# Kernel optimization log

Measured on AMD Instinct MI355X. Metric: run time of the kernel, lower is better.

The kernel has to match this reference:

```python
import jax, jax.numpy as jnp
import numpy as np

N_NODES = 50000
N_EDGES = 800000
IN_CH = 256
HID = 512
NUM_LAYERS = 3
EPS = 1e-12  # F.normalize eps


def setup_inputs() -> dict:
    key = jax.random.key(0)
    ks = jax.random.split(key, 2 + 3 * NUM_LAYERS)
    x = jax.random.normal(ks[0], (N_NODES, IN_CH), dtype=jnp.float32)
    edge_index = jax.random.randint(ks[1], (2, N_EDGES), 0, N_NODES, dtype=jnp.int64)
    inp = {"x": x, "edge_index": edge_index}
    dims = [(IN_CH, HID)] + [(HID, HID)] * (NUM_LAYERS - 1)
    for i, (din, dout) in enumerate(dims):
        s = 1.0 / np.sqrt(din)
        inp[f"Wl{i}"] = jax.random.normal(ks[2 + 3 * i], (din, dout), dtype=jnp.float32) * s
        inp[f"bl{i}"] = jnp.zeros((dout,), dtype=jnp.float32)
        inp[f"Wr{i}"] = jax.random.normal(ks[3 + 3 * i], (din, dout), dtype=jnp.float32) * s
    return inp


def _sage_conv(x, src, dst, Wl, bl, Wr):
    # aggr='add': out[dst] += x[src], then lin_l(agg) + lin_r(x), L2 normalize rows
    agg = jax.ops.segment_sum(x[src], dst, num_segments=x.shape[0])  # [N, din]
    out = agg @ Wl + bl + x @ Wr  # [N, dout]
    norm = jnp.maximum(jnp.linalg.norm(out, axis=-1, keepdims=True), EPS)
    return out / norm


def reference(x, edge_index, Wl0, bl0, Wr0, Wl1, bl1, Wr1, Wl2, bl2, Wr2):
    src, dst = edge_index[0], edge_index[1]
    feat = x
    params = [(Wl0, bl0, Wr0), (Wl1, bl1, Wr1), (Wl2, bl2, Wr2)]
    for Wl, bl, Wr in params:
        aggre = _sage_conv(feat, src, dst, Wl, bl, Wr)
        # Dropout(p=0.15) is identity in eval mode
        feat = jax.nn.elu(aggre)
    return feat
```

## Files before the change

### kernel.cpp

```cpp
#include <hip/hip_runtime.h>
#include <math.h>

#define N_NODES 50000
#define M_PAD   50048
#define N_EDGES 800000
#define HID 512

typedef short bf16x8 __attribute__((ext_vector_type(8)));
typedef float f32x4  __attribute__((ext_vector_type(4)));
typedef unsigned short u16x4 __attribute__((ext_vector_type(4)));

__device__ inline float b2f(unsigned short u) {
    union { unsigned int i; float f; } v; v.i = ((unsigned int)u) << 16; return v.f;
}
__device__ inline unsigned short f2b(float f) {
    union { float f; unsigned int i; } v; v.f = f;
    unsigned int r = v.i + 0x7FFFu + ((v.i >> 16) & 1u);
    return (unsigned short)(r >> 16);
}


__global__ void zero_kernel(int* __restrict__ p, int n) {
    int i = blockIdx.x * blockDim.x + threadIdx.x;
    if (i < n) p[i] = 0;
}

__global__ void detect_kernel(const int* __restrict__ e, int* __restrict__ flag) {
    if (blockIdx.x == 0 && threadIdx.x == 0) {
        int is64 = 1;
        for (int i = 0; i < 16; ++i)
            if (e[2 * i + 1] != 0) is64 = 0;
        *flag = is64;
    }
}

__global__ void hist_kernel(const void* __restrict__ eidx, const int* __restrict__ flag,
                            int* __restrict__ counts) {
    int e = blockIdx.x * blockDim.x + threadIdx.x;
    if (e >= N_EDGES) return;
    int is64 = *flag;
    int d;
    if (is64) d = (int)((const long long*)eidx)[N_EDGES + e];
    else      d = ((const int*)eidx)[N_EDGES + e];
    atomicAdd(&counts[d], 1);
}

__global__ __launch_bounds__(1024) void scan_kernel(const int* __restrict__ counts,
                                                    int* __restrict__ offsets) {
    __shared__ int sums[1024];
    int t = threadIdx.x;
    const int CH = (N_NODES + 1023) / 1024;
    int lo = t * CH;
    int hi = min(lo + CH, N_NODES);
    int s = 0;
    for (int i = lo; i < hi; ++i) s += counts[i];
    sums[t] = s;
    __syncthreads();
    for (int off = 1; off < 1024; off <<= 1) {
        int v = 0;
        if (t >= off) v = sums[t - off];
        __syncthreads();
        sums[t] += v;
        __syncthreads();
    }
    int excl = (t == 0) ? 0 : sums[t - 1];
    for (int i = lo; i < hi; ++i) { offsets[i] = excl; excl += counts[i]; }
    if (t == 1023) offsets[N_NODES] = excl;
}

__global__ void fill_kernel(const void* __restrict__ eidx, const int* __restrict__ flag,
                            const int* __restrict__ offsets, int* __restrict__ cursor,
                            int* __restrict__ edge_src) {
    int e = blockIdx.x * blockDim.x + threadIdx.x;
    if (e >= N_EDGES) return;
    int is64 = *flag;
    int s, d;
    if (is64) {
        const long long* p = (const long long*)eidx;
        s = (int)p[e];
        d = (int)p[N_EDGES + e];
    } else {
        const int* p = (const int*)eidx;
        s = p[e];
        d = p[N_EDGES + e];
    }
    int pos = atomicAdd(&cursor[d], 1);
    edge_src[offsets[d] + pos] = s;
}


__global__ __launch_bounds__(256) void xconv_kernel(const float* __restrict__ x,
                                                    unsigned short* __restrict__ cat1) {
    int id = blockIdx.x * 256 + threadIdx.x;
    if (id >= M_PAD * 64) return;
    int row = id >> 6;
    int c = (id & 63) * 4;
    float4 v = make_float4(0.f, 0.f, 0.f, 0.f);
    if (row < N_NODES) v = *(const float4*)(x + (size_t)row * 256 + c);
    ushort4 h;
    h.x = f2b(v.x); h.y = f2b(v.y); h.z = f2b(v.z); h.w = f2b(v.w);
    *(ushort4*)(cat1 + (size_t)row * 512 + 256 + c) = h;
}

__global__ __launch_bounds__(128) void wconv_kernel(const float* __restrict__ W,
                                                    unsigned short* __restrict__ T,
                                                    int K, int ktot, int off) {
    int n = blockIdx.x;
    for (int k = threadIdx.x; k < K; k += 128)
        T[(size_t)n * ktot + off + k] = f2b(W[(size_t)k * HID + n]);
}


template <int EPL>
__global__ __launch_bounds__(256) void aggregate_kernel(const unsigned short* __restrict__ Fh,
                                                        const int* __restrict__ off,
                                                        const int* __restrict__ esrc,
                                                        unsigned short* __restrict__ Ah) {
    const int W = EPL * 64;
    const int STRIDE = 2 * W;
    const int wid = threadIdx.x >> 6;
    const int lane = threadIdx.x & 63;
    const int node = blockIdx.x * 4 + wid;
    if (node >= N_NODES) return;
    const int beg = off[node], end = off[node + 1];
    const int deg = end - beg;

    float a0[EPL], a1[EPL];
#pragma unroll
    for (int j = 0; j < EPL; ++j) { a0[j] = 0.f; a1[j] = 0.f; }

    int idxv = (beg + lane < end) ? esrc[beg + lane] : 0;
    for (int i = 0; i < deg; i += 2) {
        const int b = i & 63;
        if (b == 0 && i)
            idxv = (beg + i + lane < end) ? esrc[beg + i + lane] : 0;
        {
            const int s = __shfl(idxv, b);
            const unsigned short* r = Fh + (size_t)s * STRIDE + lane * EPL;
#pragma unroll
            for (int q = 0; q < EPL / 4; ++q) {
                u16x4 v = *(const u16x4*)(r + q * 4);
#pragma unroll
                for (int j = 0; j < 4; ++j) a0[q * 4 + j] += b2f(v[j]);
            }
        }
        if (i + 1 < deg) {
            const int s = __shfl(idxv, b + 1);
            const unsigned short* r = Fh + (size_t)s * STRIDE + lane * EPL;
#pragma unroll
            for (int q = 0; q < EPL / 4; ++q) {
                u16x4 v = *(const u16x4*)(r + q * 4);
#pragma unroll
                for (int j = 0; j < 4; ++j) a1[q * 4 + j] += b2f(v[j]);
            }
        }
    }

    unsigned short* op = Ah + (size_t)node * STRIDE + lane * EPL;
#pragma unroll
    for (int q = 0; q < EPL / 4; ++q) {
        u16x4 h;
#pragma unroll
        for (int j = 0; j < 4; ++j) h[j] = f2b(a0[q * 4 + j] + a1[q * 4 + j]);
        *(u16x4*)(op + q * 4) = h;
    }
}


__global__ __launch_bounds__(256, 4) void gemm_mfma_kernel(
    const unsigned short* __restrict__ A, const unsigned short* __restrict__ B,
    const float* __restrict__ bias, float* __restrict__ out, int K) {
    __shared__ unsigned short S[2 * 8192];
    const int bm = blockIdx.y * 128;
    const int bn = blockIdx.x * 128;
    const int tid = threadIdx.x;
    const int l = tid & 63;
    const int w = tid >> 6;
    const int wr = (w >> 1) * 64;
    const int wc = (w & 1) * 64;
    const int arow = l >> 2;
    const int acol = (l & 3) * 8;

    const unsigned short* gA = A + (size_t)(bm + arow) * K + acol;
    const unsigned short* gB = B + (size_t)(bn + arow) * K + acol;

    f32x4 acc[4][4];
#pragma unroll
    for (int m = 0; m < 4; ++m)
#pragma unroll
        for (int n = 0; n < 4; ++n) acc[m][n] = (f32x4){0.f, 0.f, 0.f, 0.f};

    const int aoff = (wr + (l & 15)) * 32 + (l >> 4) * 8;
    const int woff = (wc + (l & 15)) * 32 + (l >> 4) * 8;
    const int ktiles = K >> 5;

    auto STAGE = [&](int buf, int kt) {
        unsigned short* lb = &S[buf * 8192];
#pragma unroll
        for (int i = 0; i < 2; ++i) {
            const int c = w * 2 + i;
            __builtin_amdgcn_global_load_lds(
                (const __attribute__((address_space(1))) void*)(gA + (size_t)(c * 16) * K + kt * 32),
                (__attribute__((address_space(3))) void*)(lb + c * 512), 16, 0, 0);
            __builtin_amdgcn_global_load_lds(
                (const __attribute__((address_space(1))) void*)(gB + (size_t)(c * 16) * K + kt * 32),
                (__attribute__((address_space(3))) void*)(lb + 4096 + c * 512), 16, 0, 0);
        }
    };

    STAGE(0, 0);
    __syncthreads();

    for (int kt = 0; kt < ktiles; ++kt) {
        if (kt + 1 < ktiles) STAGE((kt + 1) & 1, kt + 1);
        const int sb = (kt & 1) * 8192;

        bf16x8 af[4], wf[4];
#pragma unroll
        for (int m = 0; m < 4; ++m)
            af[m] = *(const bf16x8*)&S[sb + aoff + m * 512];
#pragma unroll
        for (int n = 0; n < 4; ++n)
            wf[n] = *(const bf16x8*)&S[sb + 4096 + woff + n * 512];
#pragma unroll
        for (int m = 0; m < 4; ++m)
#pragma unroll
            for (int n = 0; n < 4; ++n)
                acc[m][n] = __builtin_amdgcn_mfma_f32_16x16x32_bf16(af[m], wf[n], acc[m][n], 0, 0, 0);
        __syncthreads();
    }

    const int r0 = bm + wr + (l >> 4) * 4;
    const int c0 = bn + wc + (l & 15);
#pragma unroll
    for (int n = 0; n < 4; ++n) {
        const float bv = bias[c0 + n * 16];
#pragma unroll
        for (int m = 0; m < 4; ++m) {
#pragma unroll
            for (int j = 0; j < 4; ++j) {
                int gr = r0 + m * 16 + j;
                if (gr < N_NODES)
                    out[(size_t)gr * HID + c0 + n * 16] = acc[m][n][j] + bv;
            }
        }
    }
}


template <int FINAL>
__global__ __launch_bounds__(256) void norm_elu_kernel(const float* __restrict__ in,
                                                       float* __restrict__ outF,
                                                       unsigned short* __restrict__ Fh) {
    const int wid = threadIdx.x >> 6;
    const int lane = threadIdx.x & 63;
    const int row = blockIdx.x * 4 + wid;
    if (row >= N_NODES) return;
    const float* p = in + (size_t)row * HID + lane * 8;
    float4 v0 = *(const float4*)p;
    float4 v1 = *(const float4*)(p + 4);
    float ss = v0.x * v0.x + v0.y * v0.y + v0.z * v0.z + v0.w * v0.w
             + v1.x * v1.x + v1.y * v1.y + v1.z * v1.z + v1.w * v1.w;
#pragma unroll
    for (int o = 32; o > 0; o >>= 1) ss += __shfl_xor(ss, o);
    float inv = 1.f / fmaxf(sqrtf(ss), 1e-12f);
    float r[8] = {v0.x, v0.y, v0.z, v0.w, v1.x, v1.y, v1.z, v1.w};
#pragma unroll
    for (int j = 0; j < 8; ++j) {
        r[j] *= inv;
        r[j] = r[j] > 0.f ? r[j] : expm1f(r[j]);
    }
    if (FINAL) {
        float* q = outF + (size_t)row * HID + lane * 8;
        *(float4*)q = make_float4(r[0], r[1], r[2], r[3]);
        *(float4*)(q + 4) = make_float4(r[4], r[5], r[6], r[7]);
    } else {
        unsigned short* q = Fh + (size_t)row * 1024 + lane * 8;
        u16x4 h0, h1;
#pragma unroll
        for (int j = 0; j < 4; ++j) { h0[j] = f2b(r[j]); h1[j] = f2b(r[4 + j]); }
        *(u16x4*)q = h0;
        *(u16x4*)(q + 4) = h1;
    }
}


extern "C" void kernel_launch(void* const* d_in, const int* in_sizes, int n_in,
                              void* d_out, int out_size, void* d_ws, size_t ws_size,
                              hipStream_t stream) {
    const float* x    = (const float*)d_in[0];
    const void*  eidx = d_in[1];
    const float* Wl0 = (const float*)d_in[2];
    const float* bl0 = (const float*)d_in[3];
    const float* Wr0 = (const float*)d_in[4];
    const float* Wl1 = (const float*)d_in[5];
    const float* bl1 = (const float*)d_in[6];
    const float* Wr1 = (const float*)d_in[7];
    const float* Wl2 = (const float*)d_in[8];
    const float* bl2 = (const float*)d_in[9];
    const float* Wr2 = (const float*)d_in[10];
    float* outF = (float*)d_out;

    char* ws = (char*)d_ws;
    size_t o = 0;
    auto alloc = [&](size_t bytes) { void* p = ws + o; o += (bytes + 255) & ~(size_t)255; return p; };

    unsigned short* Cat1 = (unsigned short*)alloc((size_t)M_PAD * 512 * 2);
    unsigned short* Cat2 = (unsigned short*)alloc((size_t)M_PAD * 1024 * 2);

    unsigned short* Wcat0 = (unsigned short*)alloc(512 * 512 * 2);
    unsigned short* Wcat1 = (unsigned short*)alloc(512 * 1024 * 2);
    unsigned short* Wcat2 = (unsigned short*)alloc(512 * 1024 * 2);

    int* counts   = (int*)alloc((size_t)2 * N_NODES * 4);
    int* cursor   = counts + N_NODES;
    int* offsets  = (int*)alloc((size_t)(N_NODES + 1) * 4);
    int* edge_src = (int*)alloc((size_t)N_EDGES * 4);
    int* flag     = (int*)alloc(256);

    zero_kernel<<<(2 * N_NODES + 255) / 256, 256, 0, stream>>>(counts, 2 * N_NODES);
    detect_kernel<<<1, 64, 0, stream>>>((const int*)eidx, flag);
    hist_kernel<<<(N_EDGES + 255) / 256, 256, 0, stream>>>(eidx, flag, counts);
    scan_kernel<<<1, 1024, 0, stream>>>(counts, offsets);
    fill_kernel<<<(N_EDGES + 255) / 256, 256, 0, stream>>>(eidx, flag, offsets, cursor, edge_src);

    xconv_kernel<<<(M_PAD * 64 + 255) / 256, 256, 0, stream>>>(x, Cat1);
    wconv_kernel<<<512, 128, 0, stream>>>(Wl0, Wcat0, 256, 512, 0);
    wconv_kernel<<<512, 128, 0, stream>>>(Wr0, Wcat0, 256, 512, 256);
    wconv_kernel<<<512, 128, 0, stream>>>(Wl1, Wcat1, 512, 1024, 0);
    wconv_kernel<<<512, 128, 0, stream>>>(Wr1, Wcat1, 512, 1024, 512);
    wconv_kernel<<<512, 128, 0, stream>>>(Wl2, Wcat2, 512, 1024, 0);
    wconv_kernel<<<512, 128, 0, stream>>>(Wr2, Wcat2, 512, 1024, 512);

    dim3 ggrid(4, M_PAD / 128);
    const int ngrid = (N_NODES + 3) / 4;

    aggregate_kernel<4><<<ngrid, 256, 0, stream>>>(Cat1 + 256, offsets, edge_src, Cat1);
    gemm_mfma_kernel<<<ggrid, 256, 0, stream>>>(Cat1, Wcat0, bl0, outF, 512);
    norm_elu_kernel<0><<<ngrid, 256, 0, stream>>>(outF, nullptr, Cat2 + 512);

    aggregate_kernel<8><<<ngrid, 256, 0, stream>>>(Cat2 + 512, offsets, edge_src, Cat2);
    gemm_mfma_kernel<<<ggrid, 256, 0, stream>>>(Cat2, Wcat1, bl1, outF, 1024);
    norm_elu_kernel<0><<<ngrid, 256, 0, stream>>>(outF, nullptr, Cat2 + 512);

    aggregate_kernel<8><<<ngrid, 256, 0, stream>>>(Cat2 + 512, offsets, edge_src, Cat2);
    gemm_mfma_kernel<<<ggrid, 256, 0, stream>>>(Cat2, Wcat2, bl2, outF, 1024);
    norm_elu_kernel<1><<<ngrid, 256, 0, stream>>>(outF, outF, nullptr);

    (void)in_sizes; (void)n_in; (void)out_size; (void)ws_size;
}
```

Before: 809.3 us.

## Unroll aggregation 4-wide, store bf16 GEMM output, relax GEMM pipeline waits

The aggregation loop now processes four neighbours per iteration with 16-byte vector loads and nontemporal stores, giving more loads in flight. The intermediate GEMM outputs of the first two layers are written as bf16 instead of fp32, halving the write and reread traffic in the norm/ELU pass at some precision cost. The GEMM main loop replaces __syncthreads with an explicit partial vmcnt wait and raw barriers, so the next tile's loads can overlap compute. Epilogue stores become nontemporal.

New measurement: 847.1 us. +4.7%, slower.

```diff
diff --git a/kernel.cpp b/kernel.cpp
--- a/kernel.cpp
+++ b/kernel.cpp
@@ -9,6 +9,7 @@
 typedef short bf16x8 __attribute__((ext_vector_type(8)));
 typedef float f32x4  __attribute__((ext_vector_type(4)));
 typedef unsigned short u16x4 __attribute__((ext_vector_type(4)));
+typedef unsigned short u16x8 __attribute__((ext_vector_type(8)));
 
 __device__ inline float b2f(unsigned short u) {
     union { unsigned int i; float f; } v; v.i = ((unsigned int)u) << 16; return v.f;
@@ -125,51 +126,61 @@
     const int beg = off[node], end = off[node + 1];
     const int deg = end - beg;
 
-    float a0[EPL], a1[EPL];
-#pragma unroll
-    for (int j = 0; j < EPL; ++j) { a0[j] = 0.f; a1[j] = 0.f; }
-
-    int idxv = (beg + lane < end) ? esrc[beg + lane] : 0;
-    for (int i = 0; i < deg; i += 2) {
+    float a0[EPL], a1[EPL], a2[EPL], a3[EPL];
+#pragma unroll
+    for (int j = 0; j < EPL; ++j) { a0[j] = 0.f; a1[j] = 0.f; a2[j] = 0.f; a3[j] = 0.f; }
+
+    const int lb = lane * EPL;
+    int idxv = 0;
+
+#define ACC(ARR, S)                                                         \
+    {                                                                       \
+        const unsigned short* r_ = Fh + (size_t)(S) * STRIDE + lb;          \
+        if constexpr (EPL == 8) {                                           \
+            u16x8 v_ = *(const u16x8*)r_;                                   \
+            _Pragma("unroll")                                               \
+            for (int j_ = 0; j_ < 8; ++j_) ARR[j_] += b2f(v_[j_]);          \
+        } else {                                                            \
+            u16x4 v_ = *(const u16x4*)r_;                                   \
+            _Pragma("unroll")                                               \
+            for (int j_ = 0; j_ < 4; ++j_) ARR[j_] += b2f(v_[j_]);          \
+        }                                                                   \
+    }
+
+    for (int i = 0; i < deg; i += 4) {
         const int b = i & 63;
-        if (b == 0 && i)
-            idxv = (beg + i + lane < end) ? esrc[beg + i + lane] : 0;
-        {
-            const int s = __shfl(idxv, b);
-            const unsigned short* r = Fh + (size_t)s * STRIDE + lane * EPL;
-#pragma unroll
-            for (int q = 0; q < EPL / 4; ++q) {
-                u16x4 v = *(const u16x4*)(r + q * 4);
-#pragma unroll
-                for (int j = 0; j < 4; ++j) a0[q * 4 + j] += b2f(v[j]);
-            }
-        }
-        if (i + 1 < deg) {
-            const int s = __shfl(idxv, b + 1);
-            const unsigned short* r = Fh + (size_t)s * STRIDE + lane * EPL;
-#pragma unroll
-            for (int q = 0; q < EPL / 4; ++q) {
-                u16x4 v = *(const u16x4*)(r + q * 4);
-#pragma unroll
-                for (int j = 0; j < 4; ++j) a1[q * 4 + j] += b2f(v[j]);
-            }
-        }
-    }
-
-    unsigned short* op = Ah + (size_t)node * STRIDE + lane * EPL;
-#pragma unroll
-    for (int q = 0; q < EPL / 4; ++q) {
+        if (b == 0) idxv = (beg + i + lane < end) ? esrc[beg + i + lane] : 0;
+        const int s0 = __shfl(idxv, b);
+        const int s1 = __shfl(idxv, b + 1);
+        const int s2 = __shfl(idxv, b + 2);
+        const int s3 = __shfl(idxv, b + 3);
+        ACC(a0, s0);
+        if (i + 1 < deg) ACC(a1, s1);
+        if (i + 2 < deg) ACC(a2, s2);
+        if (i + 3 < deg) ACC(a3, s3);
+    }
+#undef ACC
+
+    unsigned short* op = Ah + (size_t)node * STRIDE + lb;
+    if constexpr (EPL == 8) {
+        u16x8 h;
+#pragma unroll
+        for (int j = 0; j < 8; ++j) h[j] = f2b(a0[j] + a1[j] + a2[j] + a3[j]);
+        __builtin_nontemporal_store(h, (u16x8*)op);
+    } else {
         u16x4 h;
 #pragma unroll
-        for (int j = 0; j < 4; ++j) h[j] = f2b(a0[q * 4 + j] + a1[q * 4 + j]);
-        *(u16x4*)(op + q * 4) = h;
-    }
-}
-
-
+        for (int j = 0; j < 4; ++j) h[j] = f2b(a0[j] + a1[j] + a2[j] + a3[j]);
+        __builtin_nontemporal_store(h, (u16x4*)op);
+    }
+}
+
+
+template <int FINAL>
 __global__ __launch_bounds__(256, 4) void gemm_mfma_kernel(
     const unsigned short* __restrict__ A, const unsigned short* __restrict__ B,
-    const float* __restrict__ bias, float* __restrict__ out, int K) {
+    const float* __restrict__ bias, float* __restrict__ outF,
+    unsigned short* __restrict__ pre, int K) {
     __shared__ unsigned short S[2 * 8192];
     const int bm = blockIdx.y * 128;
     const int bn = blockIdx.x * 128;
@@ -208,13 +219,7 @@
         }
     };
 
-    STAGE(0, 0);
-    __syncthreads();
-
-    for (int kt = 0; kt < ktiles; ++kt) {
-        if (kt + 1 < ktiles) STAGE((kt + 1) & 1, kt + 1);
-        const int sb = (kt & 1) * 8192;
-
+    auto COMPUTE = [&](int sb) {
         bf16x8 af[4], wf[4];
 #pragma unroll
         for (int m = 0; m < 4; ++m)
@@ -227,8 +232,21 @@
 #pragma unroll
             for (int n = 0; n < 4; ++n)
                 acc[m][n] = __builtin_amdgcn_mfma_f32_16x16x32_bf16(af[m], wf[n], acc[m][n], 0, 0, 0);
-        __syncthreads();
-    }
+    };
+
+    STAGE(0, 0);
+    for (int kt = 0; kt < ktiles - 1; ++kt) {
+        STAGE((kt + 1) & 1, kt + 1);
+        asm volatile("s_waitcnt vmcnt(4)" ::: "memory");
+        __builtin_amdgcn_s_barrier();
+        __builtin_amdgcn_sched_barrier(0);
+        COMPUTE((kt & 1) * 8192);
+        __builtin_amdgcn_s_barrier();
+    }
+    asm volatile("s_waitcnt vmcnt(0)" ::: "memory");
+    __builtin_amdgcn_s_barrier();
+    __builtin_amdgcn_sched_barrier(0);
+    COMPUTE(((ktiles - 1) & 1) * 8192);
 
     const int r0 = bm + wr + (l >> 4) * 4;
     const int c0 = bn + wc + (l & 15);
@@ -240,8 +258,13 @@
 #pragma unroll
             for (int j = 0; j < 4; ++j) {
                 int gr = r0 + m * 16 + j;
-                if (gr < N_NODES)
-                    out[(size_t)gr * HID + c0 + n * 16] = acc[m][n][j] + bv;
+                if (gr < N_NODES) {
+                    float val = acc[m][n][j] + bv;
+                    if constexpr (FINAL)
+                        __builtin_nontemporal_store(val, &outF[(size_t)gr * HID + c0 + n * 16]);
+                    else
+                        __builtin_nontemporal_store(f2b(val), &pre[(size_t)gr * HID + c0 + n * 16]);
+                }
             }
         }
     }
@@ -249,38 +272,47 @@
 
 
 template <int FINAL>
-__global__ __launch_bounds__(256) void norm_elu_kernel(const float* __restrict__ in,
+__global__ __launch_bounds__(256) void norm_elu_kernel(const void* __restrict__ inp,
                                                        float* __restrict__ outF,
                                                        unsigned short* __restrict__ Fh) {
     const int wid = threadIdx.x >> 6;
     const int lane = threadIdx.x & 63;
     const int row = blockIdx.x * 4 + wid;
     if (row >= N_NODES) return;
-    const float* p = in + (size_t)row * HID + lane * 8;
-    float4 v0 = *(const float4*)p;
-    float4 v1 = *(const float4*)(p + 4);
-    float ss = v0.x * v0.x + v0.y * v0.y + v0.z * v0.z + v0.w * v0.w
-             + v1.x * v1.x + v1.y * v1.y + v1.z * v1.z + v1.w * v1.w;
+    float r[8];
+    if constexpr (FINAL) {
+        const float* p = (const float*)inp + (size_t)row * HID + lane * 8;
+        float4 v0 = *(const float4*)p;
+        float4 v1 = *(const float4*)(p + 4);
+        r[0] = v0.x; r[1] = v0.y; r[2] = v0.z; r[3] = v0.w;
+        r[4] = v1.x; r[5] = v1.y; r[6] = v1.z; r[7] = v1.w;
+    } else {
+        const unsigned short* p = (const unsigned short*)inp + (size_t)row * HID + lane * 8;
+        u16x8 v = *(const u16x8*)p;
+#pragma unroll
+        for (int j = 0; j < 8; ++j) r[j] = b2f(v[j]);
+    }
+    float ss = 0.f;
+#pragma unroll
+    for (int j = 0; j < 8; ++j) ss += r[j] * r[j];
 #pragma unroll
     for (int o = 32; o > 0; o >>= 1) ss += __shfl_xor(ss, o);
     float inv = 1.f / fmaxf(sqrtf(ss), 1e-12f);
-    float r[8] = {v0.x, v0.y, v0.z, v0.w, v1.x, v1.y, v1.z, v1.w};
 #pragma unroll
     for (int j = 0; j < 8; ++j) {
         r[j] *= inv;
         r[j] = r[j] > 0.f ? r[j] : expm1f(r[j]);
     }
-    if (FINAL) {
+    if constexpr (FINAL) {
         float* q = outF + (size_t)row * HID + lane * 8;
         *(float4*)q = make_float4(r[0], r[1], r[2], r[3]);
         *(float4*)(q + 4) = make_float4(r[4], r[5], r[6], r[7]);
     } else {
         unsigned short* q = Fh + (size_t)row * 1024 + lane * 8;
-        u16x4 h0, h1;
-#pragma unroll
-        for (int j = 0; j < 4; ++j) { h0[j] = f2b(r[j]); h1[j] = f2b(r[4 + j]); }
-        *(u16x4*)q = h0;
-        *(u16x4*)(q + 4) = h1;
+        u16x8 h;
+#pragma unroll
+        for (int j = 0; j < 8; ++j) h[j] = f2b(r[j]);
+        *(u16x8*)q = h;
     }
 }
 
@@ -300,6 +332,7 @@
     const float* bl2 = (const float*)d_in[9];
     const float* Wr2 = (const float*)d_in[10];
     float* outF = (float*)d_out;
+    unsigned short* preB = (unsigned short*)d_out;
 
     char* ws = (char*)d_ws;
     size_t o = 0;
@@ -336,15 +369,15 @@
     const int ngrid = (N_NODES + 3) / 4;
 
     aggregate_kernel<4><<<ngrid, 256, 0, stream>>>(Cat1 + 256, offsets, edge_src, Cat1);
-    gemm_mfma_kernel<<<ggrid, 256, 0, stream>>>(Cat1, Wcat0, bl0, outF, 512);
-    norm_elu_kernel<0><<<ngrid, 256, 0, stream>>>(outF, nullptr, Cat2 + 512);
+    gemm_mfma_kernel<0><<<ggrid, 256, 0, stream>>>(Cat1, Wcat0, bl0, nullptr, preB, 512);
+    norm_elu_kernel<0><<<ngrid, 256, 0, stream>>>(preB, nullptr, Cat2 + 512);
 
     aggregate_kernel<8><<<ngrid, 256, 0, stream>>>(Cat2 + 512, offsets, edge_src, Cat2);
-    gemm_mfma_kernel<<<ggrid, 256, 0, stream>>>(Cat2, Wcat1, bl1, outF, 1024);
-    norm_elu_kernel<0><<<ngrid, 256, 0, stream>>>(outF, nullptr, Cat2 + 512);
+    gemm_mfma_kernel<0><<<ggrid, 256, 0, stream>>>(Cat2, Wcat1, bl1, nullptr, preB, 1024);
+    norm_elu_kernel<0><<<ngrid, 256, 0, stream>>>(preB, nullptr, Cat2 + 512);
 
     aggregate_kernel<8><<<ngrid, 256, 0, stream>>>(Cat2 + 512, offsets, edge_src, Cat2);
-    gemm_mfma_kernel<<<ggrid, 256, 0, stream>>>(Cat2, Wcat2, bl2, outF, 1024);
+    gemm_mfma_kernel<1><<<ggrid, 256, 0, stream>>>(Cat2, Wcat2, bl2, outF, nullptr, 1024);
     norm_elu_kernel<1><<<ngrid, 256, 0, stream>>>(outF, outF, nullptr);
 
     (void)in_sizes; (void)n_in; (void)out_size; (void)ws_size;
```
